# Optimization experiments

Measured on AMD Instinct MI355X. Metric: run time of the kernel, lower is better.

## Reference

```python
import jax, jax.numpy as jnp
import numpy as np

N, E = 100000, 1280000
IN_D, FEAT, HID, OUT = 256, 64, 64, 64
NEG_SLOPE = 0.2


def _gat_conv(x, src, dst, w, a_s, a_d, b, n):
    # x: [N, in], w: [in, out], a_s/a_d/b: [out]; edges src->dst (messages flow to dst)
    h = x @ w                                   # [N, out]
    e = jax.nn.leaky_relu((h @ a_s)[src] + (h @ a_d)[dst], NEG_SLOPE)  # [E]
    m = jax.ops.segment_max(e, dst, num_segments=n)                     # scatter-softmax (stable)
    ex = jnp.exp(e - m[dst])
    den = jax.ops.segment_sum(ex, dst, num_segments=n)
    alpha = ex / (den[dst] + 1e-16)
    out = jax.ops.segment_sum(alpha[:, None] * h[src], dst, num_segments=n)
    return out + b


def setup_inputs() -> dict:
    key = jax.random.key(0)
    ks = jax.random.split(key, 16)
    rn = lambda k, shape, s=0.05: jax.random.normal(k, shape, jnp.float32) * s
    return {
        'x': jax.random.normal(ks[0], (N, IN_D), jnp.float32),
        'src': jax.random.randint(ks[1], (E,), 0, N),
        'dst': jax.random.randint(ks[2], (E,), 0, N),
        'lin_w': rn(ks[3], (IN_D, FEAT)), 'lin_b': jnp.zeros((FEAT,), jnp.float32),
        'w1': rn(ks[4], (FEAT, HID)), 'a1s': rn(ks[5], (HID,)), 'a1d': rn(ks[6], (HID,)), 'b1': jnp.zeros((HID,), jnp.float32),
        'w2': rn(ks[7], (HID, HID)), 'a2s': rn(ks[8], (HID,)), 'a2d': rn(ks[9], (HID,)), 'b2': jnp.zeros((HID,), jnp.float32),
        'w3': rn(ks[10], (HID, OUT)), 'a3s': rn(ks[11], (OUT,)), 'a3d': rn(ks[12], (OUT,)), 'b3': jnp.zeros((OUT,), jnp.float32),
    }


def reference(x, src, dst, lin_w, lin_b, w1, a1s, a1d, b1, w2, a2s, a2d, b2, w3, a3s, a3d, b3):
    n = x.shape[0]
    loop = jnp.arange(n, dtype=src.dtype)        # GATConv add_self_loops=True
    s = jnp.concatenate([src, loop])
    d = jnp.concatenate([dst, loop])
    h = x @ lin_w + lin_b                        # feature_pre linear
    h = jax.nn.relu(_gat_conv(h, s, d, w1, a1s, a1d, b1, n))  # dropout is identity in eval
    h = jax.nn.relu(_gat_conv(h, s, d, w2, a2s, a2d, b2, n))
    h = _gat_conv(h, s, d, w3, a3s, a3d, b3, n)
    norm = jnp.linalg.norm(h, axis=-1, keepdims=True)          # F.normalize(p=2, dim=-1)
    return h / jnp.maximum(norm, 1e-12)
```

## Files before the change

kernel.cpp:

```cpp
#include <hip/hip_runtime.h>


constexpr float NEG_SLOPE = 0.2f;
constexpr float LOG2E = 1.4426950408889634f;
#define BKT_SHIFT 9
#define BKT_N     512
#define PCHUNK    2048
#define SRC_BITS  17

typedef __attribute__((ext_vector_type(8))) short bf16x8;
typedef __attribute__((ext_vector_type(4))) float f32x4;

__device__ inline ushort f2bf(float x) {
    union { float f; uint u; } v; v.f = x;
    return (ushort)((v.u + 0x7FFFu + ((v.u >> 16) & 1u)) >> 16);
}
__device__ inline void bf2f(uint u, float& lo, float& hi) {
    union { uint u; float f; } a, b;
    a.u = u << 16; b.u = u & 0xFFFF0000u;
    lo = a.f; hi = b.f;
}
__device__ inline uint pk(float a, float b) {
    return (uint)f2bf(a) | ((uint)f2bf(b) << 16);
}

struct PreArgs {
    const float* x; const ushort* lwT; const float* lin_b;
    const ushort* w1T; const float* a1s; const float* a1d;
    ushort* C; float* hs; float* hd; int M;
};

__global__ __launch_bounds__(256) void prep_w(
    const float* __restrict__ lw, const float* __restrict__ w1,
    const float* __restrict__ w2, const float* __restrict__ w3,
    const float* __restrict__ a2s, const float* __restrict__ a2d,
    const float* __restrict__ a3s, const float* __restrict__ a3d,
    ushort* __restrict__ lwT, ushort* __restrict__ w1T,
    ushort* __restrict__ w2T, ushort* __restrict__ w3T,
    float* __restrict__ wvec,
    int* __restrict__ cnt, int* __restrict__ ticket, int n)
{
    const int i = blockIdx.x * 256 + threadIdx.x;
    if (i < n) cnt[i] = 0;
    if (i == 0) *ticket = 0;
    if (i < 64 * 256) {
        const int nn = i >> 8, k = i & 255;
        lwT[i] = f2bf(lw[k * 64 + nn]);
    } else if (i < 64 * 256 + 4096) {
        const int j = i - 64 * 256;
        const int nn = j >> 6, k = j & 63;
        w1T[j] = f2bf(w1[k * 64 + nn]);
        w2T[j] = f2bf(w2[k * 64 + nn]);
        w3T[j] = f2bf(w3[k * 64 + nn]);
    } else if (i < 64 * 256 + 4096 + 256) {
        const int j = i - 64 * 256 - 4096;
        const int p = j >> 6, k = j & 63;
        const float* Wp = (p < 2) ? w2 : w3;
        const float* vp = (p == 0) ? a2s : (p == 1) ? a2d : (p == 2) ? a3s : a3d;
        float s = 0.f;
        #pragma unroll
        for (int t = 0; t < 64; ++t) s += Wp[k * 64 + t] * vp[t];
        wvec[p * 64 + k] = s * LOG2E;
    }
}

__device__ __forceinline__ void gemm_pre_fused(const PreArgs& pa, int tile)
{
    __shared__ __align__(16) ushort ldsA[4][8][16][8];
    __shared__ __align__(16) ushort ctile[4][16][64];
    const int tid = threadIdx.x;
    const int w = tid >> 6, lane = tid & 63;
    const int rw0 = (tile * 4 + w) * 16;
    if (rw0 >= pa.M) return;
    const int c = lane & 15, q = lane >> 4;

    const float* ap = pa.x + (size_t)(rw0 + c) * 256 + q * 8;
    float4 pv[16];
    #pragma unroll
    for (int s = 0; s < 8; ++s) {
        pv[2 * s]     = *(const float4*)(ap + s * 32);
        pv[2 * s + 1] = *(const float4*)(ap + s * 32 + 4);
    }
    f32x4 acc[4];
    #pragma unroll
    for (int t = 0; t < 4; ++t) acc[t] = (f32x4){0.f, 0.f, 0.f, 0.f};
    #pragma unroll
    for (int s = 0; s < 8; ++s) {
        const float4 p0 = pv[2 * s];
        const float4 p1 = pv[2 * s + 1];
        bf16x8 af;
        af[0] = (short)f2bf(p0.x); af[1] = (short)f2bf(p0.y);
        af[2] = (short)f2bf(p0.z); af[3] = (short)f2bf(p0.w);
        af[4] = (short)f2bf(p1.x); af[5] = (short)f2bf(p1.y);
        af[6] = (short)f2bf(p1.z); af[7] = (short)f2bf(p1.w);
        #pragma unroll
        for (int t = 0; t < 4; ++t) {
            const bf16x8 bf = *(const bf16x8*)(pa.lwT + (size_t)(t * 16 + c) * 256 + s * 32 + q * 8);
            acc[t] = __builtin_amdgcn_mfma_f32_16x16x32_bf16(af, bf, acc[t], 0, 0, 0);
        }
    }
    #pragma unroll
    for (int t = 0; t < 4; ++t) {
        const float bv = pa.lin_b[t * 16 + c];
        const int kb = 2 * t + (c >> 3);
        const int e  = c & 7;
        #pragma unroll
        for (int r = 0; r < 4; ++r)
            ldsA[w][kb][q * 4 + r][e] = f2bf(acc[t][r] + bv);
    }

    const bf16x8 a0 = *(const bf16x8*)&ldsA[w][q][c][0];
    const bf16x8 a1 = *(const bf16x8*)&ldsA[w][q + 4][c][0];
    f32x4 acc2[4];
    #pragma unroll
    for (int t = 0; t < 4; ++t) {
        const ushort* bp = pa.w1T + (size_t)(t * 16 + c) * 64 + q * 8;
        const bf16x8 b0 = *(const bf16x8*)(bp);
        const bf16x8 b1 = *(const bf16x8*)(bp + 32);
        f32x4 a = (f32x4){0.f, 0.f, 0.f, 0.f};
        a = __builtin_amdgcn_mfma_f32_16x16x32_bf16(a0, b0, a, 0, 0, 0);
        a = __builtin_amdgcn_mfma_f32_16x16x32_bf16(a1, b1, a, 0, 0, 0);
        acc2[t] = a;
    }
    float ps[4] = {0.f, 0.f, 0.f, 0.f}, pd[4] = {0.f, 0.f, 0.f, 0.f};
    #pragma unroll
    for (int t = 0; t < 4; ++t) {
        const float as = pa.a1s[t * 16 + c], ad = pa.a1d[t * 16 + c];
        #pragma unroll
        for (int r = 0; r < 4; ++r) {
            ps[r] = fmaf(acc2[t][r], as, ps[r]);
            pd[r] = fmaf(acc2[t][r], ad, pd[r]);
        }
    }
    #pragma unroll
    for (int r = 0; r < 4; ++r) {
        #pragma unroll
        for (int off = 1; off < 16; off <<= 1) {
            ps[r] += __shfl_xor(ps[r], off);
            pd[r] += __shfl_xor(pd[r], off);
        }
    }
    if (c == 0) {
        #pragma unroll
        for (int r = 0; r < 4; ++r) {
            pa.hs[rw0 + q * 4 + r] = ps[r] * LOG2E;
            pa.hd[rw0 + q * 4 + r] = pd[r] * LOG2E;
        }
    }
    #pragma unroll
    for (int t = 0; t < 4; ++t)
        #pragma unroll
        for (int r = 0; r < 4; ++r)
            ctile[w][q * 4 + r][t * 16 + c] = f2bf(acc2[t][r]);
    const int row = lane >> 2, eo = (lane & 3) * 16;
    const uint4 v0 = *(const uint4*)(&ctile[w][row][eo]);
    const uint4 v1 = *(const uint4*)(&ctile[w][row][eo + 8]);
    *(uint4*)(pa.C + (size_t)(rw0 + row) * 64 + eo)     = v0;
    *(uint4*)(pa.C + (size_t)(rw0 + row) * 64 + eo + 8) = v1;
}

__global__ __launch_bounds__(256) void edge_hist(
    const int* __restrict__ dst, int* __restrict__ cnt, int e)
{
    const int i0 = (blockIdx.x * 256 + threadIdx.x) * 4;
    if (i0 + 3 < e) {
        const int4 d = *(const int4*)(dst + i0);
        atomicAdd(&cnt[d.x], 1); atomicAdd(&cnt[d.y], 1);
        atomicAdd(&cnt[d.z], 1); atomicAdd(&cnt[d.w], 1);
    } else {
        for (int k = i0; k < e; ++k) atomicAdd(&cnt[dst[k]], 1);
    }
}

__global__ __launch_bounds__(256) void scan1_tiles(
    const int* __restrict__ cnt, int* __restrict__ out,
    int* __restrict__ bsum, int* __restrict__ ticket, int n, int nblk,
    PreArgs pa, int tile0)
{
    __shared__ int wsum[4];
    __shared__ int amLastS;
    if ((int)blockIdx.x >= nblk) {
        gemm_pre_fused(pa, tile0 + (int)blockIdx.x - nblk);
        return;
    }
    const int tid  = threadIdx.x;
    const int lane = tid & 63;
    const int w    = tid >> 6;
    const int base = blockIdx.x * 1024;
    int vals[4];
    int tsum = 0;
    #pragma unroll
    for (int i = 0; i < 4; ++i) {
        const int idx = base + tid * 4 + i;
        vals[i] = (idx < n) ? cnt[idx] : 0;
        tsum += vals[i];
    }
    int x1 = tsum;
    #pragma unroll
    for (int off = 1; off < 64; off <<= 1) {
        const int y = __shfl_up(x1, off);
        if (lane >= off) x1 += y;
    }
    if (lane == 63) wsum[w] = x1;
    __syncthreads();
    int wofs = 0;
    for (int k = 0; k < w; ++k) wofs += wsum[k];
    int excl = wofs + x1 - tsum;
    #pragma unroll
    for (int i = 0; i < 4; ++i) {
        const int idx = base + tid * 4 + i;
        if (idx < n) out[idx] = excl;
        excl += vals[i];
    }
    if (tid == 255) {
        bsum[blockIdx.x] = wofs + x1;
        __threadfence();
        amLastS = (atomicAdd(ticket, 1) == nblk - 1) ? 1 : 0;
    }
    __syncthreads();
    if (amLastS) {
        __threadfence();
        const int v2 = (tid < nblk) ? bsum[tid] : 0;
        int x2 = v2;
        #pragma unroll
        for (int off = 1; off < 64; off <<= 1) {
            const int y = __shfl_up(x2, off);
            if (lane >= off) x2 += y;
        }
        if (lane == 63) wsum[w] = x2;
        __syncthreads();
        int c2 = 0;
        for (int k = 0; k < w; ++k) c2 += wsum[k];
        if (tid < nblk) bsum[tid] = c2 + x2 - v2;
    }
}

__global__ __launch_bounds__(256) void scan3_tiles(
    int* __restrict__ out, const int* __restrict__ bsum,
    int* __restrict__ gcur, int n, int total, int s3b,
    PreArgs pa, int tile0)
{
    if ((int)blockIdx.x >= s3b) {
        gemm_pre_fused(pa, tile0 + (int)blockIdx.x - s3b);
        return;
    }
    const int idx = blockIdx.x * 256 + threadIdx.x;
    if (idx < n) {
        const int v = out[idx] + bsum[idx >> 10];
        out[idx] = v;
        if ((idx & (BKT_N - 1)) == 0) gcur[idx >> BKT_SHIFT] = v;
    }
    if (idx == 0) out[n] = total;
}

__global__ __launch_bounds__(256) void part_tiles(
    const int* __restrict__ src, const int* __restrict__ dst,
    int* __restrict__ gcursor, int* __restrict__ pairs, int e, int nb, int pb,
    PreArgs pa, int tile0)
{
    __shared__ int stage[PCHUNK];
    __shared__ unsigned char sbkt[PCHUNK];
    __shared__ int lcnt[256];
    __shared__ int lstart[256];
    __shared__ int lfill[256];
    __shared__ int gbase[256];
    __shared__ int wsum[4];

    if ((int)blockIdx.x >= pb) {
        gemm_pre_fused(pa, tile0 + (int)blockIdx.x - pb);
        return;
    }

    const int tid  = threadIdx.x;
    const int lane = tid & 63;
    const int w    = tid >> 6;
    const int base = blockIdx.x * PCHUNK;
    const int cnt_here = min(PCHUNK, e - base);

    lcnt[tid] = 0; lfill[tid] = 0;
    __syncthreads();

    for (int i = tid; i < cnt_here; i += 256)
        atomicAdd(&lcnt[dst[base + i] >> BKT_SHIFT], 1);
    __syncthreads();

    const int v = lcnt[tid];
    int x1 = v;
    #pragma unroll
    for (int off = 1; off < 64; off <<= 1) {
        const int y = __shfl_up(x1, off);
        if (lane >= off) x1 += y;
    }
    if (lane == 63) wsum[w] = x1;
    __syncthreads();
    int carry = 0;
    for (int k = 0; k < w; ++k) carry += wsum[k];
    lstart[tid] = carry + x1 - v;
    if (tid < nb && v > 0) gbase[tid] = atomicAdd(&gcursor[tid], v);
    __syncthreads();

    for (int i = tid; i < cnt_here; i += 256) {
        const int d = dst[base + i];
        const int s = src[base + i];
        const int b = d >> BKT_SHIFT;
        const int p = lstart[b] + atomicAdd(&lfill[b], 1);
        stage[p] = ((d & (BKT_N - 1)) << SRC_BITS) | s;
        sbkt[p]  = (unsigned char)b;
    }
    __syncthreads();

    for (int t = tid; t < cnt_here; t += 256) {
        const int b = sbkt[t];
        pairs[gbase[b] + (t - lstart[b])] = stage[t];
    }
}

__global__ __launch_bounds__(256) void scat_tiles(
    const int* __restrict__ pairs, const int* __restrict__ offs,
    int* __restrict__ ssrc, int n, int sb,
    PreArgs pa, int tile0)
{
    __shared__ int pos[BKT_N];
    if ((int)blockIdx.x >= sb) {
        gemm_pre_fused(pa, tile0 + (int)blockIdx.x - sb);
        return;
    }
    const int node0 = blockIdx.x << BKT_SHIFT;
    const int node1 = min(n, node0 + BKT_N);
    const int tid = threadIdx.x;
    for (int i = tid; i < node1 - node0; i += 256) pos[i] = offs[node0 + i];
    __syncthreads();
    const int e0 = offs[node0];
    const int e1 = offs[node1];
    for (int j = e0 + tid; j < e1; j += 256) {
        const int pr = pairs[j];
        const int p = atomicAdd(&pos[pr >> SRC_BITS], 1);
        ssrc[p] = pr & ((1 << SRC_BITS) - 1);
    }
}

__global__ __launch_bounds__(256) void fused_ag(
    const ushort* __restrict__ hp, const float* __restrict__ hsIn,
    const float* __restrict__ hdIn, const int* __restrict__ offs,
    const int* __restrict__ ssrc, const float* __restrict__ bias,
    const ushort* __restrict__ WT, const float* __restrict__ waS,
    const float* __restrict__ waD,
    ushort* __restrict__ C, float* __restrict__ hsOut, float* __restrict__ hdOut,
    int n)
{
    __shared__ __align__(16) ushort ldsA[8][16][8];
    __shared__ __align__(16) ushort ldsC[16][68];
    const int tid  = threadIdx.x;
    const int w    = tid >> 6, lane = tid & 63;
    const int rw0  = blockIdx.x * 16;
    const int sub  = lane >> 3;
    const int f0   = (lane & 7) * 8;

    const float4 bv0 = *(const float4*)(bias + f0);
    const float4 bv1 = *(const float4*)(bias + f0 + 4);
    const float bb[8] = {bv0.x, bv0.y, bv0.z, bv0.w, bv1.x, bv1.y, bv1.z, bv1.w};
    float ws8[8], wd8[8];
    {
        const float4 s0 = *(const float4*)(waS + f0);
        const float4 s1 = *(const float4*)(waS + f0 + 4);
        const float4 d0 = *(const float4*)(waD + f0);
        const float4 d1 = *(const float4*)(waD + f0 + 4);
        ws8[0]=s0.x; ws8[1]=s0.y; ws8[2]=s0.z; ws8[3]=s0.w;
        ws8[4]=s1.x; ws8[5]=s1.y; ws8[6]=s1.z; ws8[7]=s1.w;
        wd8[0]=d0.x; wd8[1]=d0.y; wd8[2]=d0.z; wd8[3]=d0.w;
        wd8[4]=d1.x; wd8[5]=d1.y; wd8[6]=d1.z; wd8[7]=d1.w;
    }

    #pragma unroll 1
    for (int i = 0; i < 4; ++i) {
        const int rowIdx = w * 4 + i;
        const int node = rw0 + rowIdx;
        if (node < n) {
            const int start = offs[node];
            const int end   = offs[node + 1];
            const float hdi = hdIn[node];

            int j = start + sub;
            bool vC = j < end;
            bool vN = j + 8 < end;
            int sC = vC ? ssrc[j]     : node;
            int sN = vN ? ssrc[j + 8] : sC;

            float den = 0.f;
            float acc[8] = {};
            if (sub == 0) {
                const uint4 t = *(const uint4*)(hp + (((uint)node << 6) + f0));
                float e = hsIn[node] + hdi;
                e = (e > 0.f) ? e : NEG_SLOPE * e;
                const float ex = exp2f(e);
                float f[8];
                bf2f(t.x, f[0], f[1]); bf2f(t.y, f[2], f[3]);
                bf2f(t.z, f[4], f[5]); bf2f(t.w, f[6], f[7]);
                den = ex;
                #pragma unroll
                for (int k = 0; k < 8; ++k) acc[k] = ex * f[k];
            }

            float hsC = hsIn[sC];
            uint4 tC  = *(const uint4*)(hp + (((uint)sC << 6) + f0));

            while (vC) {
                const bool vNN = j + 16 < end;
                const int  sNN = vNN ? ssrc[j + 16] : sN;
                const float hsN = hsIn[sN];
                const uint4 tN  = *(const uint4*)(hp + (((uint)sN << 6) + f0));

                float e2 = hsC + hdi;
                e2 = (e2 > 0.f) ? e2 : NEG_SLOPE * e2;
                const float ex2 = exp2f(e2);
                float f[8];
                bf2f(tC.x, f[0], f[1]); bf2f(tC.y, f[2], f[3]);
                bf2f(tC.z, f[4], f[5]); bf2f(tC.w, f[6], f[7]);
                den += ex2;
                #pragma unroll
                for (int k = 0; k < 8; ++k) acc[k] = fmaf(ex2, f[k], acc[k]);

                vC = vN; vN = vNN; sC = sN; sN = sNN; hsC = hsN; tC = tN;
                j += 8;
            }
            #pragma unroll
            for (int off = 8; off < 64; off <<= 1) {
                den += __shfl_xor(den, off);
                #pragma unroll
                for (int k = 0; k < 8; ++k) acc[k] += __shfl_xor(acc[k], off);
            }
            const float inv = 1.f / (den + 1e-16f);
            float v[8];
            #pragma unroll
            for (int k = 0; k < 8; ++k)
                v[k] = fmaxf(acc[k] * inv + bb[k], 0.f);
            float psum = 0.f, pdum = 0.f;
            #pragma unroll
            for (int k = 0; k < 8; ++k) {
                psum = fmaf(v[k], ws8[k], psum);
                pdum = fmaf(v[k], wd8[k], pdum);
            }
            #pragma unroll
            for (int off = 1; off < 8; off <<= 1) {
                psum += __shfl_xor(psum, off);
                pdum += __shfl_xor(pdum, off);
            }
            if (lane == 0) { hsOut[node] = psum; hdOut[node] = pdum; }
            if (sub == 0) {
                uint4 o;
                o.x = pk(v[0], v[1]); o.y = pk(v[2], v[3]);
                o.z = pk(v[4], v[5]); o.w = pk(v[6], v[7]);
                *(uint4*)&ldsA[lane & 7][rowIdx][0] = o;
            }
        } else if (sub == 0) {
            const uint4 z = {0u, 0u, 0u, 0u};
            *(uint4*)&ldsA[lane & 7][rowIdx][0] = z;
        }
    }
    __syncthreads();

    const int c = lane & 15, q = lane >> 4;
    const bf16x8 a0 = *(const bf16x8*)&ldsA[q][c][0];
    const bf16x8 a1 = *(const bf16x8*)&ldsA[q + 4][c][0];
    const ushort* bp = WT + (size_t)(w * 16 + c) * 64 + q * 8;
    const bf16x8 b0 = *(const bf16x8*)(bp);
    const bf16x8 b1 = *(const bf16x8*)(bp + 32);
    f32x4 a = (f32x4){0.f, 0.f, 0.f, 0.f};
    a = __builtin_amdgcn_mfma_f32_16x16x32_bf16(a0, b0, a, 0, 0, 0);
    a = __builtin_amdgcn_mfma_f32_16x16x32_bf16(a1, b1, a, 0, 0, 0);
    #pragma unroll
    for (int r = 0; r < 4; ++r)
        ldsC[q * 4 + r][w * 16 + c] = f2bf(a[r]);
    __syncthreads();

    const int row = tid >> 4, co = (tid & 15) * 4;
    if (rw0 + row < n)
        *(uint2*)(C + (size_t)(rw0 + row) * 64 + co) = *(const uint2*)&ldsC[row][co];
}

__global__ __launch_bounds__(256) void gat_agg_final(
    const ushort* __restrict__ hp, const float* __restrict__ hs,
    const float* __restrict__ hd, const int* __restrict__ offs,
    const int* __restrict__ ssrc, const float* __restrict__ bias,
    float* __restrict__ outp, int n)
{
    const int wid  = (blockIdx.x * blockDim.x + threadIdx.x) >> 6;
    const int lane = threadIdx.x & 63;
    if (wid >= n) return;
    const int sub = lane >> 3;
    const int f0  = (lane & 7) * 8;

    const int start = offs[wid];
    const int end   = offs[wid + 1];
    const float hdi = hd[wid];

    int j = start + sub;
    bool vC = j < end;
    bool vN = j + 8 < end;
    int sC = vC ? ssrc[j]     : wid;
    int sN = vN ? ssrc[j + 8] : sC;

    float den = 0.f;
    float acc[8] = {};
    if (sub == 0) {
        const uint4 t = *(const uint4*)(hp + (((uint)wid << 6) + f0));
        float e = hs[wid] + hdi;
        e = (e > 0.f) ? e : NEG_SLOPE * e;
        const float ex = exp2f(e);
        float f[8];
        bf2f(t.x, f[0], f[1]); bf2f(t.y, f[2], f[3]);
        bf2f(t.z, f[4], f[5]); bf2f(t.w, f[6], f[7]);
        den = ex;
        #pragma unroll
        for (int i = 0; i < 8; ++i) acc[i] = ex * f[i];
    }

    float hsC = hs[sC];
    uint4 tC  = *(const uint4*)(hp + (((uint)sC << 6) + f0));

    while (vC) {
        const bool vNN = j + 16 < end;
        const int  sNN = vNN ? ssrc[j + 16] : sN;
        const float hsN = hs[sN];
        const uint4 tN  = *(const uint4*)(hp + (((uint)sN << 6) + f0));

        float e2 = hsC + hdi;
        e2 = (e2 > 0.f) ? e2 : NEG_SLOPE * e2;
        const float ex2 = exp2f(e2);
        float f[8];
        bf2f(tC.x, f[0], f[1]); bf2f(tC.y, f[2], f[3]);
        bf2f(tC.z, f[4], f[5]); bf2f(tC.w, f[6], f[7]);
        den += ex2;
        #pragma unroll
        for (int i = 0; i < 8; ++i) acc[i] = fmaf(ex2, f[i], acc[i]);

        vC = vN; vN = vNN; sC = sN; sN = sNN; hsC = hsN; tC = tN;
        j += 8;
    }
    #pragma unroll
    for (int off = 8; off < 64; off <<= 1) {
        den += __shfl_xor(den, off);
        #pragma unroll
        for (int i = 0; i < 8; ++i) acc[i] += __shfl_xor(acc[i], off);
    }
    const float4 bv0 = *(const float4*)(bias + f0);
    const float4 bv1 = *(const float4*)(bias + f0 + 4);
    const float bb[8] = {bv0.x, bv0.y, bv0.z, bv0.w, bv1.x, bv1.y, bv1.z, bv1.w};
    const float inv = 1.f / (den + 1e-16f);
    float v[8];
    #pragma unroll
    for (int i = 0; i < 8; ++i) v[i] = acc[i] * inv + bb[i];
    float sq = 0.f;
    #pragma unroll
    for (int i = 0; i < 8; ++i) sq += v[i] * v[i];
    #pragma unroll
    for (int off = 1; off < 8; off <<= 1) sq += __shfl_xor(sq, off);
    const float s = 1.f / fmaxf(sqrtf(sq), 1e-12f);
    if (sub == 0) {
        float* op = outp + (size_t)wid * 64 + f0;
        float4 o0, o1;
        o0.x = v[0] * s; o0.y = v[1] * s; o0.z = v[2] * s; o0.w = v[3] * s;
        o1.x = v[4] * s; o1.y = v[5] * s; o1.z = v[6] * s; o1.w = v[7] * s;
        *(float4*)(op)     = o0;
        *(float4*)(op + 4) = o1;
    }
}

extern "C" void kernel_launch(void* const* d_in, const int* in_sizes, int n_in,
                              void* d_out, int out_size, void* d_ws, size_t ws_size,
                              hipStream_t stream)
{
    const float* x     = (const float*)d_in[0];
    const int*   src   = (const int*)d_in[1];
    const int*   dst   = (const int*)d_in[2];
    const float* lin_w = (const float*)d_in[3];
    const float* lin_b = (const float*)d_in[4];
    const float* w1  = (const float*)d_in[5];
    const float* a1s = (const float*)d_in[6];
    const float* a1d = (const float*)d_in[7];
    const float* b1  = (const float*)d_in[8];
    const float* w2  = (const float*)d_in[9];
    const float* a2s = (const float*)d_in[10];
    const float* a2d = (const float*)d_in[11];
    const float* b2  = (const float*)d_in[12];
    const float* w3  = (const float*)d_in[13];
    const float* a3s = (const float*)d_in[14];
    const float* a3d = (const float*)d_in[15];
    const float* b3  = (const float*)d_in[16];

    const int n = in_sizes[0] / 256;
    const int E = in_sizes[1];
    const int nb = (n + BKT_N - 1) >> BKT_SHIFT;

    char* wsp = (char*)d_ws;
    auto alloc = [&](size_t bytes) -> void* {
        void* p = (void*)wsp;
        wsp += (bytes + 255) & ~(size_t)255;
        return p;
    };
    ushort* bufA = (ushort*)alloc((size_t)n * 64 * sizeof(ushort));
    ushort* bufB = (ushort*)alloc((size_t)n * 64 * sizeof(ushort));
    float*  hsA  = (float*)alloc((size_t)n * sizeof(float));
    float*  hdA  = (float*)alloc((size_t)n * sizeof(float));
    float*  hsB  = (float*)alloc((size_t)n * sizeof(float));
    float*  hdB  = (float*)alloc((size_t)n * sizeof(float));
    int*    offs = (int*)alloc((size_t)(n + 1) * sizeof(int));
    int*    cnt  = (int*)alloc((size_t)n * sizeof(int));
    int*    bsum = (int*)alloc(1024 * sizeof(int));
    int*    gcur = (int*)alloc(256 * sizeof(int));
    int*    tick = (int*)alloc(256 * sizeof(int));
    int*    ssrc = (int*)alloc((size_t)E * sizeof(int));
    int*    pairs = (int*)alloc((size_t)E * sizeof(int));
    ushort* lwT = (ushort*)alloc(64 * 256 * sizeof(ushort));
    ushort* w1T = (ushort*)alloc(64 * 64 * sizeof(ushort));
    ushort* w2T = (ushort*)alloc(64 * 64 * sizeof(ushort));
    ushort* w3T = (ushort*)alloc(64 * 64 * sizeof(ushort));
    float*  wvec = (float*)alloc(256 * sizeof(float));

    const int gemmBlocks = (n + 63) / 64;
    const int nScanBlocks = (n + 1023) / 1024;
    const int s3Blocks = (n + 255) / 256;
    const int histBlocks = (E / 4 + 255) / 256 + 1;
    const int partBlocks = (E + PCHUNK - 1) / PCHUNK;
    const int fusedBlocks = (n + 15) / 16;
    const int aggBlocks = (n + 3) / 4;

    const int TA = 200;
    const int TB = 300;
    const int TC = 400;
    const int TD = gemmBlocks - TA - TB - TC;

    PreArgs pa{x, lwT, lin_b, w1T, a1s, a1d, bufB, hsB, hdB, n};

    prep_w<<<(n + 255) / 256, 256, 0, stream>>>(
        lin_w, w1, w2, w3, a2s, a2d, a3s, a3d,
        lwT, w1T, w2T, w3T, wvec, cnt, tick, n);
    edge_hist<<<histBlocks, 256, 0, stream>>>(dst, cnt, E);
    scan1_tiles<<<nScanBlocks + TA, 256, 0, stream>>>(
        cnt, offs, bsum, tick, n, nScanBlocks, pa, 0);
    scan3_tiles<<<s3Blocks + TB, 256, 0, stream>>>(
        offs, bsum, gcur, n, E, s3Blocks, pa, TA);
    part_tiles<<<partBlocks + TC, 256, 0, stream>>>(
        src, dst, gcur, pairs, E, nb, partBlocks, pa, TA + TB);
    scat_tiles<<<nb + TD, 256, 0, stream>>>(
        pairs, offs, ssrc, n, nb, pa, TA + TB + TC);

    fused_ag<<<fusedBlocks, 256, 0, stream>>>(
        bufB, hsB, hdB, offs, ssrc, b1, w2T, wvec, wvec + 64,
        bufA, hsA, hdA, n);
    fused_ag<<<fusedBlocks, 256, 0, stream>>>(
        bufA, hsA, hdA, offs, ssrc, b2, w3T, wvec + 128, wvec + 192,
        bufB, hsB, hdB, n);
    gat_agg_final<<<aggBlocks, 256, 0, stream>>>(
        bufB, hsB, hdB, offs, ssrc, b3, (float*)d_out, n);
}
```

Before: 472.3 us.

## Replace per-node histogram and global scan with bucket-level counts and local CSR offsets

Swaps the per-node atomic histogram, the two-pass global scan and the zeroing of a per-node count array for a bucket-level histogram, counted in shared memory and then added to 256 global counters. Per-node offsets are now computed inside each bucket's scatter block with a local count and scan over the bucket's pairs. This removes one kernel launch, the heavy global atomics over 1.28M edges, and the node-sized scan traffic, but the scatter blocks now read their pairs twice.

```diff
diff --git a/kernel.cpp b/kernel.cpp
--- a/kernel.cpp
+++ b/kernel.cpp
@@ -38,10 +38,10 @@
     ushort* __restrict__ lwT, ushort* __restrict__ w1T,
     ushort* __restrict__ w2T, ushort* __restrict__ w3T,
     float* __restrict__ wvec,
-    int* __restrict__ cnt, int* __restrict__ ticket, int n)
+    int* __restrict__ bcnt, int* __restrict__ ticket)
 {
     const int i = blockIdx.x * 256 + threadIdx.x;
-    if (i < n) cnt[i] = 0;
+    if (i < 256) bcnt[i] = 0;
     if (i == 0) *ticket = 0;
     if (i < 64 * 256) {
         const int nn = i >> 8, k = i & 255;
@@ -159,98 +159,53 @@
     *(uint4*)(pa.C + (size_t)(rw0 + row) * 64 + eo + 8) = v1;
 }
 
-__global__ __launch_bounds__(256) void edge_hist(
-    const int* __restrict__ dst, int* __restrict__ cnt, int e)
-{
-    const int i0 = (blockIdx.x * 256 + threadIdx.x) * 4;
-    if (i0 + 3 < e) {
-        const int4 d = *(const int4*)(dst + i0);
-        atomicAdd(&cnt[d.x], 1); atomicAdd(&cnt[d.y], 1);
-        atomicAdd(&cnt[d.z], 1); atomicAdd(&cnt[d.w], 1);
-    } else {
-        for (int k = i0; k < e; ++k) atomicAdd(&cnt[dst[k]], 1);
-    }
-}
-
-__global__ __launch_bounds__(256) void scan1_tiles(
-    const int* __restrict__ cnt, int* __restrict__ out,
-    int* __restrict__ bsum, int* __restrict__ ticket, int n, int nblk,
-    PreArgs pa, int tile0)
-{
+__global__ __launch_bounds__(256) void bhist_tiles(
+    const int* __restrict__ dst, int* __restrict__ bcnt,
+    int* __restrict__ bbase, int* __restrict__ gcur, int* __restrict__ ticket,
+    int e, int nb, int nchunks, PreArgs pa, int tile0)
+{
+    __shared__ int lcnt[256];
     __shared__ int wsum[4];
     __shared__ int amLastS;
-    if ((int)blockIdx.x >= nblk) {
-        gemm_pre_fused(pa, tile0 + (int)blockIdx.x - nblk);
+    if ((int)blockIdx.x >= nchunks) {
+        gemm_pre_fused(pa, tile0 + (int)blockIdx.x - nchunks);
         return;
     }
     const int tid  = threadIdx.x;
     const int lane = tid & 63;
     const int w    = tid >> 6;
-    const int base = blockIdx.x * 1024;
-    int vals[4];
-    int tsum = 0;
-    #pragma unroll
-    for (int i = 0; i < 4; ++i) {
-        const int idx = base + tid * 4 + i;
-        vals[i] = (idx < n) ? cnt[idx] : 0;
-        tsum += vals[i];
-    }
-    int x1 = tsum;
-    #pragma unroll
-    for (int off = 1; off < 64; off <<= 1) {
-        const int y = __shfl_up(x1, off);
-        if (lane >= off) x1 += y;
-    }
-    if (lane == 63) wsum[w] = x1;
-    __syncthreads();
-    int wofs = 0;
-    for (int k = 0; k < w; ++k) wofs += wsum[k];
-    int excl = wofs + x1 - tsum;
-    #pragma unroll
-    for (int i = 0; i < 4; ++i) {
-        const int idx = base + tid * 4 + i;
-        if (idx < n) out[idx] = excl;
-        excl += vals[i];
-    }
-    if (tid == 255) {
-        bsum[blockIdx.x] = wofs + x1;
+    const int base = blockIdx.x * PCHUNK;
+    const int cnt_here = min(PCHUNK, e - base);
+
+    lcnt[tid] = 0;
+    __syncthreads();
+    for (int i = tid; i < cnt_here; i += 256)
+        atomicAdd(&lcnt[dst[base + i] >> BKT_SHIFT], 1);
+    __syncthreads();
+    if (tid < nb && lcnt[tid] > 0) atomicAdd(&bcnt[tid], lcnt[tid]);
+    __syncthreads();
+    if (tid == 0) {
         __threadfence();
-        amLastS = (atomicAdd(ticket, 1) == nblk - 1) ? 1 : 0;
+        amLastS = (atomicAdd(ticket, 1) == nchunks - 1) ? 1 : 0;
     }
     __syncthreads();
     if (amLastS) {
         __threadfence();
-        const int v2 = (tid < nblk) ? bsum[tid] : 0;
-        int x2 = v2;
+        const int v = (tid < nb) ? bcnt[tid] : 0;
+        int x1 = v;
         #pragma unroll
         for (int off = 1; off < 64; off <<= 1) {
-            const int y = __shfl_up(x2, off);
-            if (lane >= off) x2 += y;
+            const int y = __shfl_up(x1, off);
+            if (lane >= off) x1 += y;
         }
-        if (lane == 63) wsum[w] = x2;
+        if (lane == 63) wsum[w] = x1;
         __syncthreads();
-        int c2 = 0;
-        for (int k = 0; k < w; ++k) c2 += wsum[k];
-        if (tid < nblk) bsum[tid] = c2 + x2 - v2;
-    }
-}
-
-__global__ __launch_bounds__(256) void scan3_tiles(
-    int* __restrict__ out, const int* __restrict__ bsum,
-    int* __restrict__ gcur, int n, int total, int s3b,
-    PreArgs pa, int tile0)
-{
-    if ((int)blockIdx.x >= s3b) {
-        gemm_pre_fused(pa, tile0 + (int)blockIdx.x - s3b);
-        return;
-    }
-    const int idx = blockIdx.x * 256 + threadIdx.x;
-    if (idx < n) {
-        const int v = out[idx] + bsum[idx >> 10];
-        out[idx] = v;
-        if ((idx & (BKT_N - 1)) == 0) gcur[idx >> BKT_SHIFT] = v;
-    }
-    if (idx == 0) out[n] = total;
+        int carry = 0;
+        for (int k = 0; k < w; ++k) carry += wsum[k];
+        const int excl = carry + x1 - v;
+        if (tid < nb) { bbase[tid] = excl; gcur[tid] = excl; }
+        if (tid == 0) bbase[nb] = e;
+    }
 }
 
 __global__ __launch_bounds__(256) void part_tiles(
@@ -316,25 +271,57 @@
 }
 
 __global__ __launch_bounds__(256) void scat_tiles(
-    const int* __restrict__ pairs, const int* __restrict__ offs,
-    int* __restrict__ ssrc, int n, int sb,
+    const int* __restrict__ pairs, const int* __restrict__ bbase,
+    int* __restrict__ offs, int* __restrict__ ssrc, int n, int nb,
     PreArgs pa, int tile0)
 {
-    __shared__ int pos[BKT_N];
-    if ((int)blockIdx.x >= sb) {
-        gemm_pre_fused(pa, tile0 + (int)blockIdx.x - sb);
+    __shared__ int lcnt[BKT_N];
+    __shared__ int lofs[BKT_N];
+    __shared__ int wsum[4];
+    if ((int)blockIdx.x >= nb) {
+        gemm_pre_fused(pa, tile0 + (int)blockIdx.x - nb);
         return;
     }
-    const int node0 = blockIdx.x << BKT_SHIFT;
-    const int node1 = min(n, node0 + BKT_N);
-    const int tid = threadIdx.x;
-    for (int i = tid; i < node1 - node0; i += 256) pos[i] = offs[node0 + i];
-    __syncthreads();
-    const int e0 = offs[node0];
-    const int e1 = offs[node1];
+    const int b     = blockIdx.x;
+    const int tid   = threadIdx.x;
+    const int lane  = tid & 63;
+    const int w     = tid >> 6;
+    const int node0 = b << BKT_SHIFT;
+    const int nlocal = min(n - node0, BKT_N);
+    const int e0 = bbase[b];
+    const int e1 = bbase[b + 1];
+
+    lcnt[tid] = 0; lcnt[tid + 256] = 0;
+    __syncthreads();
+
+    for (int j = e0 + tid; j < e1; j += 256)
+        atomicAdd(&lcnt[pairs[j] >> SRC_BITS], 1);
+    __syncthreads();
+
+    const int v0 = lcnt[2 * tid], v1 = lcnt[2 * tid + 1];
+    const int tsum = v0 + v1;
+    int x1 = tsum;
+    #pragma unroll
+    for (int off = 1; off < 64; off <<= 1) {
+        const int y = __shfl_up(x1, off);
+        if (lane >= off) x1 += y;
+    }
+    if (lane == 63) wsum[w] = x1;
+    __syncthreads();
+    int carry = 0;
+    for (int k = 0; k < w; ++k) carry += wsum[k];
+    const int excl = carry + x1 - tsum;
+    lofs[2 * tid]     = e0 + excl;
+    lofs[2 * tid + 1] = e0 + excl + v0;
+    __syncthreads();
+
+    for (int i = tid; i < nlocal; i += 256) offs[node0 + i] = lofs[i];
+    if (b == nb - 1 && tid == 0) offs[n] = e1;
+    __syncthreads();
+
     for (int j = e0 + tid; j < e1; j += 256) {
         const int pr = pairs[j];
-        const int p = atomicAdd(&pos[pr >> SRC_BITS], 1);
+        const int p = atomicAdd(&lofs[pr >> SRC_BITS], 1);
         ssrc[p] = pr & ((1 << SRC_BITS) - 1);
     }
 }
@@ -605,8 +592,8 @@
     float*  hsB  = (float*)alloc((size_t)n * sizeof(float));
     float*  hdB  = (float*)alloc((size_t)n * sizeof(float));
     int*    offs = (int*)alloc((size_t)(n + 1) * sizeof(int));
-    int*    cnt  = (int*)alloc((size_t)n * sizeof(int));
-    int*    bsum = (int*)alloc(1024 * sizeof(int));
+    int*    bcnt = (int*)alloc(256 * sizeof(int));
+    int*    bbase = (int*)alloc(257 * sizeof(int));
     int*    gcur = (int*)alloc(256 * sizeof(int));
     int*    tick = (int*)alloc(256 * sizeof(int));
     int*    ssrc = (int*)alloc((size_t)E * sizeof(int));
@@ -618,32 +605,25 @@
     float*  wvec = (float*)alloc(256 * sizeof(float));
 
     const int gemmBlocks = (n + 63) / 64;
-    const int nScanBlocks = (n + 1023) / 1024;
-    const int s3Blocks = (n + 255) / 256;
-    const int histBlocks = (E / 4 + 255) / 256 + 1;
     const int partBlocks = (E + PCHUNK - 1) / PCHUNK;
     const int fusedBlocks = (n + 15) / 16;
     const int aggBlocks = (n + 3) / 4;
 
-    const int TA = 200;
-    const int TB = 300;
-    const int TC = 400;
-    const int TD = gemmBlocks - TA - TB - TC;
+    const int TA = 400;
+    const int TB = 500;
+    const int TC = gemmBlocks - TA - TB;
 
     PreArgs pa{x, lwT, lin_b, w1T, a1s, a1d, bufB, hsB, hdB, n};
 
-    prep_w<<<(n + 255) / 256, 256, 0, stream>>>(
+    prep_w<<<(64 * 256 + 4096 + 256 + 255) / 256, 256, 0, stream>>>(
         lin_w, w1, w2, w3, a2s, a2d, a3s, a3d,
-        lwT, w1T, w2T, w3T, wvec, cnt, tick, n);
-    edge_hist<<<histBlocks, 256, 0, stream>>>(dst, cnt, E);
-    scan1_tiles<<<nScanBlocks + TA, 256, 0, stream>>>(
-        cnt, offs, bsum, tick, n, nScanBlocks, pa, 0);
-    scan3_tiles<<<s3Blocks + TB, 256, 0, stream>>>(
-        offs, bsum, gcur, n, E, s3Blocks, pa, TA);
-    part_tiles<<<partBlocks + TC, 256, 0, stream>>>(
-        src, dst, gcur, pairs, E, nb, partBlocks, pa, TA + TB);
-    scat_tiles<<<nb + TD, 256, 0, stream>>>(
-        pairs, offs, ssrc, n, nb, pa, TA + TB + TC);
+        lwT, w1T, w2T, w3T, wvec, bcnt, tick);
+    bhist_tiles<<<partBlocks + TA, 256, 0, stream>>>(
+        dst, bcnt, bbase, gcur, tick, E, nb, partBlocks, pa, 0);
+    part_tiles<<<partBlocks + TB, 256, 0, stream>>>(
+        src, dst, gcur, pairs, E, nb, partBlocks, pa, TA);
+    scat_tiles<<<nb + TC, 256, 0, stream>>>(
+        pairs, bbase, offs, ssrc, n, nb, pa, TA + TB);
 
     fused_ag<<<fusedBlocks, 256, 0, stream>>>(
         bufB, hsB, hdB, offs, ssrc, b1, w2T, wvec, wvec + 64,
```

Result: faster. 435.9 us (-7.7%).
